# Performance work log

Hardware: AMD Instinct MI355X
Metric: run time of the kernel (lower is better)

Reference implementation:

```python
import jax, jax.numpy as jnp
import numpy as np

B, T, D = 4, 256, 512          # batch, seq_len, encoder_dim
L, H = 2, 8                    # num xLSTM blocks, num heads
I = 2 * D                      # inner dim (proj_factor=2)
DH = I // H                    # per-head dim = 128
K, G = 32, 64                  # mdn_components, goal_dim
EPS = 1e-5


def _ln(x, s, b):
    m = x.mean(-1, keepdims=True)
    v = jnp.mean((x - m) ** 2, -1, keepdims=True)
    return (x - m) * jax.lax.rsqrt(v + EPS) * s + b


def setup_inputs() -> dict:
    key = jax.random.key(0)
    ks = jax.random.split(key, 16)
    sc = 0.02
    nrm = lambda k, shp: jax.random.normal(k, shp, jnp.float32) * sc
    return {
        "x": jax.random.normal(ks[0], (B, T, D), jnp.float32),
        "ln_s": jnp.ones((L, D), jnp.float32),
        "ln_b": jnp.zeros((L, D), jnp.float32),
        "W_proj": nrm(ks[1], (L, D, 2 * I)),
        "Wq": nrm(ks[2], (L, I, I)),
        "Wk": nrm(ks[3], (L, I, I)),
        "Wv": nrm(ks[4], (L, I, I)),
        "Wi": nrm(ks[5], (L, I, H)),
        "bi": jnp.zeros((L, H), jnp.float32),
        "Wf": nrm(ks[6], (L, I, H)),
        "bf": jnp.full((L, H), 3.0, jnp.float32),  # forget-gate bias init
        "gn_s": jnp.ones((L, I), jnp.float32),
        "gn_b": jnp.zeros((L, I), jnp.float32),
        "W_down": nrm(ks[7], (L, I, D)),
        "fln_s": jnp.ones((D,), jnp.float32),
        "fln_b": jnp.zeros((D,), jnp.float32),
        "W_pi": nrm(ks[8], (D, K)),
        "b_pi": jnp.zeros((K,), jnp.float32),
        "W_mu": nrm(ks[9], (D, K * G)),
        "b_mu": jnp.zeros((K * G,), jnp.float32),
        "W_sig": nrm(ks[10], (D, K * G)),
        "b_sig": jnp.zeros((K * G,), jnp.float32),
    }


def _forward(x, ln_s, ln_b, W_proj, Wq, Wk, Wv, Wi, bi, Wf, bf,
             gn_s, gn_b, W_down, fln_s, fln_b,
             W_pi, b_pi, W_mu, b_mu, W_sig, b_sig):
    inv_sqrt_dh = 1.0 / (DH ** 0.5)

    def step(carry, x_t):  # x_t: (B, D); replicates per-timestep xlstm_stack.step()
        C, n, m = carry    # (L,B,H,DH,DH), (L,B,H,DH), (L,B,H)
        h = x_t
        for l in range(L):  # fixed small block loop
            skip = h
            xn = _ln(h, ln_s[l], ln_b[l])
            xp = xn @ W_proj[l]                      # (B, 2I)
            xm, z = jnp.split(xp, 2, axis=-1)        # mLSTM branch / gate branch
            q = (xm @ Wq[l]).reshape(B, H, DH)
            k = (xm @ Wk[l]).reshape(B, H, DH) * inv_sqrt_dh
            v = (xm @ Wv[l]).reshape(B, H, DH)
            ip = xm @ Wi[l] + bi[l]                  # (B, H) exp input gate preact
            fp = xm @ Wf[l] + bf[l]                  # (B, H) forget gate preact
            logf = jax.nn.log_sigmoid(fp)
            m_new = jnp.maximum(logf + m[l], ip)     # stabilizer
            ig = jnp.exp(ip - m_new)
            fg = jnp.exp(logf + m[l] - m_new)
            # matrix memory update: C <- f*C + i * k v^T ; n <- f*n + i*k
            C_new = fg[:, :, None, None] * C[l] + ig[:, :, None, None] * (k[..., :, None] * v[..., None, :])
            n_new = fg[..., None] * n[l] + ig[..., None] * k
            num = jnp.einsum('bhk,bhkv->bhv', q, C_new)
            den = jnp.maximum(jnp.abs(jnp.einsum('bhk,bhk->bh', q, n_new)), 1.0)
            hh = num / den[..., None]                # (B, H, DH)
            # multi-head norm (per-head layernorm, no per-head affine)
            mu_h = hh.mean(-1, keepdims=True)
            var_h = jnp.mean((hh - mu_h) ** 2, -1, keepdims=True)
            hh = (hh - mu_h) * jax.lax.rsqrt(var_h + EPS)
            hh = hh.reshape(B, I) * gn_s[l] + gn_b[l]
            hh = hh * jax.nn.silu(z)                 # output gating branch
            h = skip + hh @ W_down[l]                # residual
            C = C.at[l].set(C_new)
            n = n.at[l].set(n_new)
            m = m.at[l].set(m_new)
        return (C, n, m), h

    C0 = jnp.zeros((L, B, H, DH, DH), x.dtype)
    n0 = jnp.zeros((L, B, H, DH), x.dtype)
    m0 = jnp.zeros((L, B, H), x.dtype)
    _, hs = jax.lax.scan(step, (C0, n0, m0), jnp.swapaxes(x, 0, 1))
    last = _ln(hs[-1], fln_s, fln_b)                 # post-blocks norm on final step
    pi = jax.nn.softmax(last @ W_pi + b_pi, axis=-1)              # (B, K)
    mu = (last @ W_mu + b_mu).reshape(B, K, G)                     # (B, K, G)
    sigma = jax.nn.softplus(last @ W_sig + b_sig).reshape(B, K, G) # (B, K, G)
    return pi, mu, sigma


def reference(x, ln_s, ln_b, W_proj, Wq, Wk, Wv, Wi, bi, Wf, bf,
              gn_s, gn_b, W_down, fln_s, fln_b,
              W_pi, b_pi, W_mu, b_mu, W_sig, b_sig):
    return _forward(x, ln_s, ln_b, W_proj, Wq, Wk, Wv, Wi, bi, Wf, bf,
                    gn_s, gn_b, W_down, fln_s, fln_b,
                    W_pi, b_pi, W_mu, b_mu, W_sig, b_sig)
```

## Files before the change

### kernel.cpp

```cpp
#include <hip/hip_runtime.h>
#include <hip/hip_bf16.h>
#include <math.h>

#define DEV __device__ __forceinline__

typedef __attribute__((ext_vector_type(8))) short bf16x8;
typedef __attribute__((ext_vector_type(4))) float f32x4;

static DEV float softplus_f(float x){ return fmaxf(x,0.f) + log1pf(expf(-fabsf(x))); }
static DEV float logsig_f(float x){ return fminf(x,0.f) - log1pf(expf(-fabsf(x))); }
static DEV float silu_f(float x){ return x / (1.f + expf(-x)); }
static DEV unsigned short f2bf(float f){
  union { float f; unsigned u; } v; v.f = f;
  unsigned r = (v.u + 0x7fffu + ((v.u >> 16) & 1u)) >> 16;
  return (unsigned short)r;
}
static DEV float bf2f(unsigned short u){
  union { unsigned u; float f; } v; v.u = ((unsigned)u) << 16; return v.f;
}

__global__ void wconv_all(const float* __restrict__ Wp, const float* __restrict__ Wq,
                          const float* __restrict__ Wk, const float* __restrict__ Wv,
                          const float* __restrict__ Wd,
                          unsigned short* projT0, unsigned short* projT1,
                          unsigned short* qT0, unsigned short* kT0, unsigned short* kT1,
                          unsigned short* vT0, unsigned short* vT1, unsigned short* dT0)
{
  int z = blockIdx.z;
  const float* W; unsigned short* Wt; int K, M; float scale = 1.f;
  const float INV = 0.08838834764831845f;
  switch (z){
    case 0: W = Wp;              Wt = projT0; K = 512;  M = 2048; break;
    case 1: W = Wp + 512*2048;   Wt = projT1; K = 512;  M = 2048; break;
    case 2: W = Wq;              Wt = qT0;    K = 1024; M = 1024; break;
    case 3: W = Wk;              Wt = kT0;    K = 1024; M = 1024; scale = INV; break;
    case 4: W = Wk + 1048576;    Wt = kT1;    K = 1024; M = 1024; scale = INV; break;
    case 5: W = Wv;              Wt = vT0;    K = 1024; M = 1024; break;
    case 6: W = Wv + 1048576;    Wt = vT1;    K = 1024; M = 1024; break;
    default: W = Wd;             Wt = dT0;    K = 1024; M = 512;  break;
  }
  int m0 = blockIdx.x * 32, k0 = blockIdx.y * 32;
  if (m0 >= M || k0 >= K) return;
  __shared__ float s[32][33];
  int tx = threadIdx.x & 31, ty = threadIdx.x >> 5;
  #pragma unroll
  for (int u = 0; u < 32; u += 8)
    s[ty+u][tx] = W[(size_t)(k0+ty+u)*M + m0 + tx];
  __syncthreads();
  #pragma unroll
  for (int u = 0; u < 32; u += 8)
    Wt[(size_t)(m0+ty+u)*K + k0 + tx] = f2bf(s[tx][ty+u] * scale);
}

__global__ __launch_bounds__(256) void wcomb2(const float* __restrict__ W_proj,
                                              const float* __restrict__ Wi,
                                              const float* __restrict__ Wf,
                                              float* __restrict__ Wc)
{
  int gid = blockIdx.x * 4 + (threadIdx.x >> 6);
  int l = gid >> 9, d = gid & 511;
  int lane = threadIdx.x & 63;
  const float* wp = W_proj + (size_t)l*512*2048 + (size_t)d*2048 + lane*16;
  const float* wi = Wi + (size_t)l*1024*8;
  const float* wf = Wf + (size_t)l*1024*8;
  float acc[16];
  #pragma unroll
  for (int q = 0; q < 16; ++q) acc[q] = 0.f;
  #pragma unroll 4
  for (int u = 0; u < 16; ++u){
    float xv = wp[u];
    int j = lane*16 + u;
    float4 wi0 = *(const float4*)(wi + j*8);
    float4 wi1 = *(const float4*)(wi + j*8 + 4);
    float4 wf0 = *(const float4*)(wf + j*8);
    float4 wf1 = *(const float4*)(wf + j*8 + 4);
    acc[0]  = fmaf(xv, wi0.x, acc[0]);  acc[1]  = fmaf(xv, wi0.y, acc[1]);
    acc[2]  = fmaf(xv, wi0.z, acc[2]);  acc[3]  = fmaf(xv, wi0.w, acc[3]);
    acc[4]  = fmaf(xv, wi1.x, acc[4]);  acc[5]  = fmaf(xv, wi1.y, acc[5]);
    acc[6]  = fmaf(xv, wi1.z, acc[6]);  acc[7]  = fmaf(xv, wi1.w, acc[7]);
    acc[8]  = fmaf(xv, wf0.x, acc[8]);  acc[9]  = fmaf(xv, wf0.y, acc[9]);
    acc[10] = fmaf(xv, wf0.z, acc[10]); acc[11] = fmaf(xv, wf0.w, acc[11]);
    acc[12] = fmaf(xv, wf1.x, acc[12]); acc[13] = fmaf(xv, wf1.y, acc[13]);
    acc[14] = fmaf(xv, wf1.z, acc[14]); acc[15] = fmaf(xv, wf1.w, acc[15]);
  }
  #pragma unroll
  for (int o = 32; o > 0; o >>= 1){
    #pragma unroll
    for (int q = 0; q < 16; ++q) acc[q] += __shfl_xor(acc[q], o);
  }
  if (lane == 0){
    float* dst = Wc + (size_t)l*512*16 + d*16;
    #pragma unroll
    for (int q = 0; q < 16; ++q) dst[q] = acc[q];
  }
}

__global__ __launch_bounds__(256) void ln_gates(
    const float* __restrict__ in, unsigned short* __restrict__ outb,
    const float* __restrict__ s, const float* __restrict__ b,
    const float* __restrict__ Wc, float* __restrict__ ipfp)
{
  int r = blockIdx.x;
  const float* x = in + (size_t)r * 512;
  int tid = threadIdx.x;
  float lsum = 0.f, lsq = 0.f;
  for (int i = tid; i < 512; i += 256){ float v = x[i]; lsum += v; lsq += v*v; }
  #pragma unroll
  for (int o = 32; o > 0; o >>= 1){ lsum += __shfl_down(lsum, o); lsq += __shfl_down(lsq, o); }
  __shared__ float s1[4], s2[4];
  int wid = tid >> 6, lane = tid & 63;
  if (lane == 0){ s1[wid] = lsum; s2[wid] = lsq; }
  __syncthreads();
  if (tid == 0){ float a=0.f,c=0.f; for (int w=0; w<4; ++w){ a+=s1[w]; c+=s2[w]; } s1[0]=a; s2[0]=c; }
  __syncthreads();
  float mean = s1[0] * (1.f/512.f);
  float var  = s2[0] * (1.f/512.f) - mean*mean;
  float rstd = rsqrtf(var + 1e-5f);
  __shared__ float P[256][17];
  float g[16];
  #pragma unroll
  for (int q = 0; q < 16; ++q) g[q] = 0.f;
  for (int i = tid; i < 512; i += 256){
    float v = (x[i]-mean)*rstd*s[i] + b[i];
    outb[(size_t)r*512 + i] = f2bf(v);
    const float* wrow = Wc + i*16;
    #pragma unroll
    for (int q = 0; q < 16; ++q) g[q] = fmaf(v, wrow[q], g[q]);
  }
  #pragma unroll
  for (int q = 0; q < 16; ++q) P[tid][q] = g[q];
  __syncthreads();
  {
    int q = tid >> 4, c = tid & 15;
    float sacc = 0.f;
    #pragma unroll
    for (int u = 0; u < 16; ++u) sacc += P[c*16 + u][q];
    sacc += __shfl_xor(sacc, 1); sacc += __shfl_xor(sacc, 2);
    sacc += __shfl_xor(sacc, 4); sacc += __shfl_xor(sacc, 8);
    if (c == 0) ipfp[r*16 + q] = sacc;
  }
}

__global__ __launch_bounds__(256) void gemm_mfma128_multi(
    const unsigned short* __restrict__ A, int lda,
    const unsigned short* __restrict__ Bt0, const unsigned short* __restrict__ Bt1,
    const unsigned short* __restrict__ Bt2, int ldb,
    unsigned short* __restrict__ C0, unsigned short* __restrict__ C1,
    unsigned short* __restrict__ C2, int ldc, int K)
{
  const unsigned short* Bt = (blockIdx.z == 0) ? Bt0 : (blockIdx.z == 1) ? Bt1 : Bt2;
  unsigned short* Cbf      = (blockIdx.z == 0) ? C0  : (blockIdx.z == 1) ? C1  : C2;
  __shared__ __align__(16) unsigned short As[128][72];
  __shared__ __align__(16) unsigned short Bs[128][72];
  int row0 = blockIdx.y * 128, col0 = blockIdx.x * 128;
  int tid = threadIdx.x;
  int w = tid >> 6, l = tid & 63;
  int wr = (w >> 1) * 64, wc = (w & 1) * 64;
  int lr = l & 15, lk = l >> 4;
  f32x4 acc[4][4] = {};
  for (int k0 = 0; k0 < K; k0 += 64){
    #pragma unroll
    for (int u = 0; u < 4; ++u){
      int o = u*256 + tid, r = o >> 3, c = (o & 7) * 8;
      *(bf16x8*)&As[r][c] = *(const bf16x8*)(A  + (size_t)(row0 + r) * lda + k0 + c);
      *(bf16x8*)&Bs[r][c] = *(const bf16x8*)(Bt + (size_t)(col0 + r) * ldb + k0 + c);
    }
    __syncthreads();
    #pragma unroll
    for (int kk = 0; kk < 2; ++kk){
      bf16x8 af[4], bfr[4];
      #pragma unroll
      for (int i = 0; i < 4; ++i) af[i]  = *(const bf16x8*)&As[wr + i*16 + lr][kk*32 + lk*8];
      #pragma unroll
      for (int j = 0; j < 4; ++j) bfr[j] = *(const bf16x8*)&Bs[wc + j*16 + lr][kk*32 + lk*8];
      #pragma unroll
      for (int i = 0; i < 4; ++i)
        #pragma unroll
        for (int j = 0; j < 4; ++j)
          acc[i][j] = __builtin_amdgcn_mfma_f32_16x16x32_bf16(af[i], bfr[j], acc[i][j], 0, 0, 0);
    }
    __syncthreads();
  }
  #pragma unroll
  for (int i = 0; i < 4; ++i){
    #pragma unroll
    for (int j = 0; j < 4; ++j){
      int col = col0 + wc + j*16 + lr;
      #pragma unroll
      for (int r = 0; r < 4; ++r){
        int row = row0 + wr + i*16 + lk*4 + r;
        Cbf[(size_t)row*ldc + col] = f2bf(acc[i][j][r]);
      }
    }
  }
}

__global__ __launch_bounds__(256) void gemm_mfma(
    const unsigned short* __restrict__ A, int lda,
    const unsigned short* __restrict__ Bt, int ldb,
    float* __restrict__ C, int ldc,
    unsigned short* __restrict__ Cbf,
    const float* __restrict__ skip, int ldskip,
    int K)
{
  __shared__ __align__(16) unsigned short As[64][72];
  __shared__ __align__(16) unsigned short Bs[64][72];
  int row0 = blockIdx.y * 64, col0 = blockIdx.x * 64;
  int tid = threadIdx.x;
  int w = tid >> 6, l = tid & 63;
  int wr = (w >> 1) * 32, wc = (w & 1) * 32;
  int lr = l & 15, lk = l >> 4;
  int r1 = tid >> 3, c1 = (tid & 7) * 8;
  int r2 = (tid + 256) >> 3, c2 = ((tid + 256) & 7) * 8;
  const unsigned short* a1 = A  + (size_t)(row0 + r1) * lda + c1;
  const unsigned short* a2 = A  + (size_t)(row0 + r2) * lda + c2;
  const unsigned short* b1 = Bt + (size_t)(col0 + r1) * ldb + c1;
  const unsigned short* b2 = Bt + (size_t)(col0 + r2) * ldb + c2;
  f32x4 acc00 = {0,0,0,0}, acc01 = {0,0,0,0}, acc10 = {0,0,0,0}, acc11 = {0,0,0,0};
  for (int k0 = 0; k0 < K; k0 += 64){
    *(bf16x8*)&As[r1][c1] = *(const bf16x8*)(a1 + k0);
    *(bf16x8*)&As[r2][c2] = *(const bf16x8*)(a2 + k0);
    *(bf16x8*)&Bs[r1][c1] = *(const bf16x8*)(b1 + k0);
    *(bf16x8*)&Bs[r2][c2] = *(const bf16x8*)(b2 + k0);
    __syncthreads();
    #pragma unroll
    for (int kk = 0; kk < 2; ++kk){
      bf16x8 a0 = *(const bf16x8*)&As[wr + lr][kk*32 + lk*8];
      bf16x8 a1f = *(const bf16x8*)&As[wr + 16 + lr][kk*32 + lk*8];
      bf16x8 b0 = *(const bf16x8*)&Bs[wc + lr][kk*32 + lk*8];
      bf16x8 b1f = *(const bf16x8*)&Bs[wc + 16 + lr][kk*32 + lk*8];
      acc00 = __builtin_amdgcn_mfma_f32_16x16x32_bf16(a0, b0, acc00, 0, 0, 0);
      acc01 = __builtin_amdgcn_mfma_f32_16x16x32_bf16(a0, b1f, acc01, 0, 0, 0);
      acc10 = __builtin_amdgcn_mfma_f32_16x16x32_bf16(a1f, b0, acc10, 0, 0, 0);
      acc11 = __builtin_amdgcn_mfma_f32_16x16x32_bf16(a1f, b1f, acc11, 0, 0, 0);
    }
    __syncthreads();
  }
  #pragma unroll
  for (int i = 0; i < 2; ++i){
    #pragma unroll
    for (int j = 0; j < 2; ++j){
      f32x4 a = (i == 0) ? ((j == 0) ? acc00 : acc01) : ((j == 0) ? acc10 : acc11);
      int col = col0 + wc + j*16 + lr;
      #pragma unroll
      for (int r = 0; r < 4; ++r){
        int row = row0 + wr + i*16 + lk*4 + r;
        float o = a[r];
        if (skip) o += skip[(size_t)row*ldskip + col];
        if (C)   C[(size_t)row*ldc + col] = o;
        if (Cbf) Cbf[(size_t)row*ldc + col] = f2bf(o);
      }
    }
  }
}

__global__ void scan_gates(const float* __restrict__ ipfp,
                           const float* __restrict__ bi, const float* __restrict__ bfg,
                           float* __restrict__ alpha, float* __restrict__ Mt)
{
  int bh = blockIdx.x; int b = bh >> 3, h = bh & 7;
  int lane = threadIdx.x;
  float bih = bi[h], bfh = bfg[h];
  float lf[4], ip[4];
  #pragma unroll
  for (int u = 0; u < 4; ++u){
    int t = lane*4 + u, r = b*256 + t;
    ip[u] = ipfp[r*16 + h] + bih;
    lf[u] = logsig_f(ipfp[r*16 + 8 + h] + bfh);
  }
  float c0 = lf[0], c1 = c0+lf[1], c2 = c1+lf[2], c3 = c2+lf[3];
  float tot = c3, pre = tot;
  #pragma unroll
  for (int o = 1; o < 64; o <<= 1){ float v = __shfl_up(pre, o); if (lane >= o) pre += v; }
  float excl = pre - tot;
  float F[4] = {excl+c0, excl+c1, excl+c2, excl+c3};
  float al[4];
  #pragma unroll
  for (int u = 0; u < 4; ++u) al[u] = ip[u] - F[u];
  float lm[4];
  lm[0] = al[0]; lm[1] = fmaxf(lm[0], al[1]); lm[2] = fmaxf(lm[1], al[2]); lm[3] = fmaxf(lm[2], al[3]);
  float pm = lm[3];
  #pragma unroll
  for (int o = 1; o < 64; o <<= 1){ float v = __shfl_up(pm, o); if (lane >= o) pm = fmaxf(pm, v); }
  float pmexcl = __shfl_up(pm, 1);
  if (lane == 0) pmexcl = -3.4e38f;
  int base = bh*256 + lane*4;
  #pragma unroll
  for (int u = 0; u < 4; ++u){
    alpha[base+u] = al[u];
    Mt[base+u] = fmaxf(0.f, fmaxf(pmexcl, lm[u]));
  }
}

__global__ __launch_bounds__(256) void attn_l0_mfma(
    const unsigned short* __restrict__ q, const unsigned short* __restrict__ k,
    const unsigned short* __restrict__ v,
    const float* __restrict__ alpha, const float* __restrict__ Mt,
    const unsigned short* __restrict__ xpb,
    const float* __restrict__ gn_s, const float* __restrict__ gn_b,
    unsigned short* __restrict__ gated)
{
  __shared__ __align__(16) char smem[46080];
  unsigned short (*Ks)[136] = (unsigned short(*)[136])smem;
  unsigned short (*Vt)[72]  = (unsigned short(*)[72])(smem + 17408);
  unsigned short (*Ps)[72]  = (unsigned short(*)[72])(smem + 35840);
  float* alpha_sh = (float*)(smem + 45056);
  float* Mt_sh    = (float*)(smem + 45312);
  float (*denL)[64] = (float(*)[64])(smem + 45568);
  float (*numf)[140] = (float(*)[140])smem;

  int blk = blockIdx.x;
  int tt = blk & 3, h = (blk >> 2) & 7, b = blk >> 5;
  int t0 = tt * 64;
  int tid = threadIdx.x;
  int w = tid >> 6, l = tid & 63;
  int wr = (w >> 1) * 32;
  int wc = (w & 1) * 32;
  int wd = (w & 1) * 64;
  int lrm = l & 15, lk = l >> 4;
  int bhT = ((b*8 + h) << 8);
  size_t headoff = (size_t)h * 128;

  {
    #pragma unroll
    for (int u = 0; u < 4; ++u){
      int o = u*256 + tid, row = o >> 4, oct = o & 15;
      *(bf16x8*)&Ks[row][oct*8] =
        *(const bf16x8*)(q + (size_t)(b*256 + t0 + row)*1024 + headoff + oct*8);
    }
    if (tid < 64) Mt_sh[tid] = Mt[bhT + t0 + tid];
    if (tid < 128) ((float*)denL)[tid] = 0.f;
  }
  __syncthreads();
  bf16x8 aq[2][4];
  #pragma unroll
  for (int i = 0; i < 2; ++i)
    #pragma unroll
    for (int kk = 0; kk < 4; ++kk)
      aq[i][kk] = *(const bf16x8*)&Ks[wr + i*16 + lrm][kk*32 + lk*8];
  __syncthreads();

  f32x4 pacc[2][4] = {};
  int ntile = tt + 1;

  for (int it = 0; it < ntile; ++it){
    int s0 = it * 64;
    #pragma unroll
    for (int u = 0; u < 4; ++u){
      int o = u*256 + tid, row = o >> 4, oct = o & 15;
      *(bf16x8*)&Ks[row][oct*8] =
        *(const bf16x8*)(k + (size_t)(b*256 + s0 + row)*1024 + headoff + oct*8);
    }
    #pragma unroll
    for (int u = 0; u < 2; ++u){
      int task = u*256 + tid;
      int sp = task & 31, oct = task >> 5;
      const unsigned short* vp = v + (size_t)(b*256 + s0 + sp*2)*1024 + headoff + oct*8;
      bf16x8 r0 = *(const bf16x8*)vp;
      bf16x8 r1 = *(const bf16x8*)(vp + 1024);
      #pragma unroll
      for (int j = 0; j < 8; ++j){
        unsigned lo = (unsigned short)r0[j];
        unsigned hi = (unsigned short)r1[j];
        *(unsigned*)&Vt[oct*8 + j][sp*2] = lo | (hi << 16);
      }
    }
    if (tid < 64) alpha_sh[tid] = alpha[bhT + s0 + tid];
    __syncthreads();

    f32x4 sacc[2][2] = {};
    #pragma unroll
    for (int kk = 0; kk < 4; ++kk){
      bf16x8 b0 = *(const bf16x8*)&Ks[wc + lrm][kk*32 + lk*8];
      bf16x8 b1 = *(const bf16x8*)&Ks[wc + 16 + lrm][kk*32 + lk*8];
      sacc[0][0] = __builtin_amdgcn_mfma_f32_16x16x32_bf16(aq[0][kk], b0, sacc[0][0], 0, 0, 0);
      sacc[0][1] = __builtin_amdgcn_mfma_f32_16x16x32_bf16(aq[0][kk], b1, sacc[0][1], 0, 0, 0);
      sacc[1][0] = __builtin_amdgcn_mfma_f32_16x16x32_bf16(aq[1][kk], b0, sacc[1][0], 0, 0, 0);
      sacc[1][1] = __builtin_amdgcn_mfma_f32_16x16x32_bf16(aq[1][kk], b1, sacc[1][1], 0, 0, 0);
    }

    bool diag = (it == ntile - 1);
    float av0 = alpha_sh[wc + lrm];
    float av1 = alpha_sh[wc + 16 + lrm];
    #pragma unroll
    for (int i = 0; i < 2; ++i){
      #pragma unroll
      for (int r = 0; r < 4; ++r){
        int tl = wr + i*16 + lk*4 + r;
        float mt = Mt_sh[tl];
        float p0 = __expf(av0 - mt) * sacc[i][0][r];
        float p1 = __expf(av1 - mt) * sacc[i][1][r];
        if (diag){
          if (wc + lrm      > tl) p0 = 0.f;
          if (wc + 16 + lrm > tl) p1 = 0.f;
        }
        Ps[tl][wc + lrm]      = f2bf(p0);
        Ps[tl][wc + 16 + lrm] = f2bf(p1);
        float dv = p0 + p1;
        dv += __shfl_xor(dv, 1); dv += __shfl_xor(dv, 2);
        dv += __shfl_xor(dv, 4); dv += __shfl_xor(dv, 8);
        if (lrm == 0) denL[w & 1][tl] += dv;
      }
    }
    __syncthreads();

    #pragma unroll
    for (int ks = 0; ks < 2; ++ks){
      bf16x8 pa0 = *(const bf16x8*)&Ps[wr + lrm][ks*32 + lk*8];
      bf16x8 pa1 = *(const bf16x8*)&Ps[wr + 16 + lrm][ks*32 + lk*8];
      #pragma unroll
      for (int jd = 0; jd < 4; ++jd){
        bf16x8 vb8 = *(const bf16x8*)&Vt[wd + jd*16 + lrm][ks*32 + lk*8];
        pacc[0][jd] = __builtin_amdgcn_mfma_f32_16x16x32_bf16(pa0, vb8, pacc[0][jd], 0, 0, 0);
        pacc[1][jd] = __builtin_amdgcn_mfma_f32_16x16x32_bf16(pa1, vb8, pacc[1][jd], 0, 0, 0);
      }
    }
    __syncthreads();
  }

  #pragma unroll
  for (int i = 0; i < 2; ++i)
    #pragma unroll
    for (int jd = 0; jd < 4; ++jd)
      #pragma unroll
      for (int r = 0; r < 4; ++r)
        numf[wr + i*16 + lk*4 + r][wd + jd*16 + lrm] = pacc[i][jd][r];
  if (tid < 64){
    float s = denL[0][tid] + denL[1][tid];
    alpha_sh[tid] = 1.0f / fmaxf(fabsf(s), 1.0f);
  }
  __syncthreads();

  {
    int row = tid >> 2, qq = tid & 3;
    float inv = alpha_sh[row];
    const float* nr = &numf[row][qq*32];
    float xs[32];
    float sum = 0.f, sq = 0.f;
    #pragma unroll
    for (int j = 0; j < 8; ++j){
      float4 t4 = *(const float4*)(nr + j*4);
      float v0 = t4.x*inv, v1 = t4.y*inv, v2 = t4.z*inv, v3 = t4.w*inv;
      xs[j*4+0] = v0; xs[j*4+1] = v1; xs[j*4+2] = v2; xs[j*4+3] = v3;
      sum += v0+v1+v2+v3;
      sq  += v0*v0+v1*v1+v2*v2+v3*v3;
    }
    sum += __shfl_xor(sum, 1); sq += __shfl_xor(sq, 1);
    sum += __shfl_xor(sum, 2); sq += __shfl_xor(sq, 2);
    float mean = sum * (1.f/128.f);
    float var  = sq  * (1.f/128.f) - mean*mean;
    float rstd = rsqrtf(var + 1e-5f);
    int rr = b*256 + t0 + row;
    const unsigned short* zp = xpb + (size_t)rr*2048 + 1024 + headoff + qq*32;
    const float* gsP = gn_s + headoff + qq*32;
    const float* gbP = gn_b + headoff + qq*32;
    unsigned short* op = gated + (size_t)rr*1024 + headoff + qq*32;
    #pragma unroll
    for (int j8 = 0; j8 < 4; ++j8){
      bf16x8 zv = *(const bf16x8*)(zp + j8*8);
      bf16x8 ov;
      #pragma unroll
      for (int j = 0; j < 8; ++j){
        int jj = j8*8 + j;
        float valn = (xs[jj]-mean)*rstd*gsP[jj] + gbP[jj];
        ov[j] = (short)f2bf(valn * silu_f(bf2f((unsigned short)zv[j])));
      }
      *(bf16x8*)(op + j8*8) = ov;
    }
  }
}

__global__ void qlast_split(const unsigned short* __restrict__ xpb, const float* __restrict__ Wq1,
                            float* __restrict__ part)
{
  int jt = blockIdx.x, ks = blockIdx.y;
  int j = jt*256 + threadIdx.x;
  __shared__ float xs[4][32];
  int t = threadIdx.x;
  if (t < 128){ int b = t >> 5, kk = t & 31; xs[b][kk] = bf2f(xpb[(size_t)(b*256+255)*2048 + ks*32 + kk]); }
  __syncthreads();
  float a0=0.f,a1=0.f,a2=0.f,a3=0.f;
  #pragma unroll 8
  for (int kk = 0; kk < 32; ++kk){
    float wv = Wq1[(size_t)(ks*32+kk)*1024 + j];
    a0 = fmaf(xs[0][kk], wv, a0);
    a1 = fmaf(xs[1][kk], wv, a1);
    a2 = fmaf(xs[2][kk], wv, a2);
    a3 = fmaf(xs[3][kk], wv, a3);
  }
  part[((size_t)ks*4 + 0)*1024 + j] = a0;
  part[((size_t)ks*4 + 1)*1024 + j] = a1;
  part[((size_t)ks*4 + 2)*1024 + j] = a2;
  part[((size_t)ks*4 + 3)*1024 + j] = a3;
}

__global__ __launch_bounds__(256) void attn_l1_split(
    const float* __restrict__ qpart, const unsigned short* __restrict__ k1,
    const unsigned short* __restrict__ v1,
    const float* __restrict__ alpha, const float* __restrict__ Mt,
    float* __restrict__ pnum, float* __restrict__ pden)
{
  int sc = blockIdx.x, bh = blockIdx.y;
  int b = bh >> 3, h = bh & 7;
  int s0 = sc * 32;
  int tid = threadIdx.x;
  __shared__ float qsh[128];
  __shared__ float sred[32][9];
  __shared__ float as[32];
  __shared__ float nred[2][128];
  if (tid < 128){
    float s = 0.f;
    #pragma unroll 8
    for (int ks = 0; ks < 32; ++ks) s += qpart[((size_t)ks*4 + b)*1024 + h*128 + tid];
    qsh[tid] = s;
  }
  __syncthreads();
  {
    int sl = tid & 31, dc = tid >> 5;
    const unsigned short* kp = k1 + (size_t)(b*256 + s0 + sl)*1024 + h*128 + dc*16;
    float p = 0.f;
    #pragma unroll
    for (int u = 0; u < 16; u += 8){
      bf16x8 kv = *(const bf16x8*)(kp + u);
      #pragma unroll
      for (int e = 0; e < 8; ++e) p = fmaf(qsh[dc*16+u+e], bf2f((unsigned short)kv[e]), p);
    }
    sred[sl][dc] = p;
  }
  __syncthreads();
  if (tid < 32){
    float sum = 0.f;
    #pragma unroll
    for (int dc = 0; dc < 8; ++dc) sum += sred[tid][dc];
    float w = __expf(alpha[bh*256 + s0 + tid] - Mt[bh*256 + 255]);
    as[tid] = w * sum;
  }
  __syncthreads();
  {
    int d = tid & 127, sg = tid >> 7;
    const unsigned short* vp = v1 + (size_t)(b*256 + s0 + sg*16)*1024 + h*128 + d;
    float np = 0.f;
    #pragma unroll
    for (int u = 0; u < 16; ++u) np = fmaf(as[sg*16 + u], bf2f(vp[(size_t)u*1024]), np);
    nred[sg][d] = np;
  }
  __syncthreads();
  if (tid < 128) pnum[((size_t)bh*8 + sc)*128 + tid] = nred[0][tid] + nred[1][tid];
  if (tid == 128){
    float dsum = 0.f;
    #pragma unroll
    for (int u = 0; u < 32; ++u) dsum += as[u];
    pden[bh*8 + sc] = dsum;
  }
}

__global__ __launch_bounds__(128) void attn_l1_fin(
    const float* __restrict__ pnum, const float* __restrict__ pden,
    const unsigned short* __restrict__ xpb,
    const float* __restrict__ gn_s, const float* __restrict__ gn_b,
    float* __restrict__ gated1)
{
  int bh = blockIdx.x; int b = bh >> 3, h = bh & 7;
  int tid = threadIdx.x;
  __shared__ float hh[128];
  __shared__ float dsh, msh, rsh;
  float nsum = 0.f;
  #pragma unroll
  for (int sc = 0; sc < 8; ++sc) nsum += pnum[((size_t)bh*8 + sc)*128 + tid];
  if (tid == 0){
    float d = 0.f;
    #pragma unroll
    for (int sc = 0; sc < 8; ++sc) d += pden[bh*8 + sc];
    dsh = fmaxf(fabsf(d), 1.0f);
  }
  __syncthreads();
  float hv = nsum / dsh;
  hh[tid] = hv;
  __syncthreads();
  if (tid < 64){
    float a = hh[tid], c = hh[tid + 64];
    float s1 = a + c, s2v = a*a + c*c;
    #pragma unroll
    for (int o = 32; o > 0; o >>= 1){ s1 += __shfl_down(s1, o); s2v += __shfl_down(s2v, o); }
    if (tid == 0){
      float mean = s1*(1.f/128.f);
      float var  = s2v*(1.f/128.f) - mean*mean;
      msh = mean; rsh = rsqrtf(var + 1e-5f);
    }
  }
  __syncthreads();
  {
    int i = h*128 + tid;
    float valn = (hv - msh)*rsh*gn_s[i] + gn_b[i];
    float z = bf2f(xpb[(size_t)(b*256 + 255)*2048 + 1024 + i]);
    gated1[b*1024 + i] = valn * silu_f(z);
  }
}

__global__ void dl_split(const float* __restrict__ gated1, const float* __restrict__ Wd,
                         float* __restrict__ part)
{
  int jt = blockIdx.x, ks = blockIdx.y;
  int j = jt*256 + threadIdx.x;
  __shared__ float xs[4][32];
  int t = threadIdx.x;
  if (t < 128){ int b = t >> 5, kk = t & 31; xs[b][kk] = gated1[b*1024 + ks*32 + kk]; }
  __syncthreads();
  float a0=0.f,a1=0.f,a2=0.f,a3=0.f;
  #pragma unroll 8
  for (int kk = 0; kk < 32; ++kk){
    float wv = Wd[(size_t)(ks*32+kk)*512 + j];
    a0 = fmaf(xs[0][kk], wv, a0);
    a1 = fmaf(xs[1][kk], wv, a1);
    a2 = fmaf(xs[2][kk], wv, a2);
    a3 = fmaf(xs[3][kk], wv, a3);
  }
  part[((size_t)ks*4 + 0)*512 + j] = a0;
  part[((size_t)ks*4 + 1)*512 + j] = a1;
  part[((size_t)ks*4 + 2)*512 + j] = a2;
  part[((size_t)ks*4 + 3)*512 + j] = a3;
}

__global__ __launch_bounds__(256) void dl_fin(
    const float* __restrict__ part, const float* __restrict__ h0,
    const float* __restrict__ fln_s, const float* __restrict__ fln_b,
    float* __restrict__ lastb)
{
  int b = blockIdx.x;
  int tid = threadIdx.x;
  float v[2];
  #pragma unroll
  for (int u = 0; u < 2; ++u){
    int jj = tid*2 + u;
    float s = 0.f;
    #pragma unroll 8
    for (int ks = 0; ks < 32; ++ks) s += part[((size_t)ks*4 + b)*512 + jj];
    v[u] = h0[(size_t)(b*256 + 255)*512 + jj] + s;
  }
  float lsum = v[0] + v[1], lsq = v[0]*v[0] + v[1]*v[1];
  #pragma unroll
  for (int o = 32; o > 0; o >>= 1){ lsum += __shfl_down(lsum, o); lsq += __shfl_down(lsq, o); }
  __shared__ float s1[4], s2[4];
  int wid = tid >> 6, lane = tid & 63;
  if (lane == 0){ s1[wid] = lsum; s2[wid] = lsq; }
  __syncthreads();
  if (tid == 0){ float a=0.f,c=0.f; for (int w2=0; w2<4; ++w2){ a+=s1[w2]; c+=s2[w2]; } s1[0]=a; s2[0]=c; }
  __syncthreads();
  float mean = s1[0] * (1.f/512.f);
  float var  = s2[0] * (1.f/512.f) - mean*mean;
  float rstd = rsqrtf(var + 1e-5f);
  #pragma unroll
  for (int u = 0; u < 2; ++u){
    int jj = tid*2 + u;
    lastb[b*512 + jj] = (v[u]-mean)*rstd*fln_s[jj] + fln_b[jj];
  }
}

__global__ void ms_split(const float* __restrict__ last,
                         const float* __restrict__ W_mu, const float* __restrict__ W_sig,
                         float* __restrict__ part)
{
  int jt = blockIdx.x, ks = blockIdx.y, mat = blockIdx.z;
  int j = jt*256 + threadIdx.x;
  const float* W = mat ? W_sig : W_mu;
  __shared__ float xs[4][64];
  int t = threadIdx.x;
  { int b = t >> 6, kk = t & 63; xs[b][kk] = last[b*512 + ks*64 + kk]; }
  __syncthreads();
  float a0=0.f,a1=0.f,a2=0.f,a3=0.f;
  #pragma unroll 8
  for (int kk = 0; kk < 64; ++kk){
    float wv = W[(size_t)(ks*64+kk)*2048 + j];
    a0 = fmaf(xs[0][kk], wv, a0);
    a1 = fmaf(xs[1][kk], wv, a1);
    a2 = fmaf(xs[2][kk], wv, a2);
    a3 = fmaf(xs[3][kk], wv, a3);
  }
  size_t base = ((size_t)(mat*8 + ks)*4);
  part[(base + 0)*2048 + j] = a0;
  part[(base + 1)*2048 + j] = a1;
  part[(base + 2)*2048 + j] = a2;
  part[(base + 3)*2048 + j] = a3;
}

__global__ void ms_reduce(const float* __restrict__ part,
                          const float* __restrict__ b_mu, const float* __restrict__ b_sig,
                          float* __restrict__ out)
{
  int j = blockIdx.x*256 + threadIdx.x;
  int b = blockIdx.y, mat = blockIdx.z;
  float s = mat ? b_sig[j] : b_mu[j];
  for (int ks = 0; ks < 8; ++ks) s += part[((size_t)(mat*8 + ks)*4 + b)*2048 + j];
  out[128 + mat*8192 + b*2048 + j] = mat ? softplus_f(s) : s;
}

__global__ void heads_pi(const float* __restrict__ last,
                         const float* __restrict__ W_pi, const float* __restrict__ b_pi,
                         float* __restrict__ out)
{
  __shared__ float ls[512];
  int b = blockIdx.x, o = threadIdx.x;
  for (int i = o; i < 512; i += 64) ls[i] = last[b*512 + i];
  __syncthreads();
  bool valid = o < 32;
  float acc = -3.4e38f;
  if (valid){
    acc = b_pi[o];
    for (int i = 0; i < 512; ++i) acc = fmaf(ls[i], W_pi[i*32 + o], acc);
  }
  float m = acc;
  #pragma unroll
  for (int o2 = 32; o2 > 0; o2 >>= 1) m = fmaxf(m, __shfl_xor(m, o2));
  float e = valid ? expf(acc - m) : 0.f;
  float ssum = e;
  #pragma unroll
  for (int o2 = 32; o2 > 0; o2 >>= 1) ssum += __shfl_xor(ssum, o2);
  if (valid) out[b*32 + o] = e / ssum;
}

extern "C" void kernel_launch(void* const* d_in, const int* in_sizes, int n_in,
                              void* d_out, int out_size, void* d_ws, size_t ws_size,
                              hipStream_t stream)
{
  const float* x      = (const float*)d_in[0];
  const float* ln_s   = (const float*)d_in[1];
  const float* ln_b   = (const float*)d_in[2];
  const float* W_proj = (const float*)d_in[3];
  const float* Wq     = (const float*)d_in[4];
  const float* Wk     = (const float*)d_in[5];
  const float* Wv     = (const float*)d_in[6];
  const float* Wi     = (const float*)d_in[7];
  const float* bi     = (const float*)d_in[8];
  const float* Wf     = (const float*)d_in[9];
  const float* bf     = (const float*)d_in[10];
  const float* gn_s   = (const float*)d_in[11];
  const float* gn_b   = (const float*)d_in[12];
  const float* W_down = (const float*)d_in[13];
  const float* fln_s  = (const float*)d_in[14];
  const float* fln_b  = (const float*)d_in[15];
  const float* W_pi   = (const float*)d_in[16];
  const float* b_pi   = (const float*)d_in[17];
  const float* W_mu   = (const float*)d_in[18];
  const float* b_mu   = (const float*)d_in[19];
  const float* W_sig  = (const float*)d_in[20];
  const float* b_sig  = (const float*)d_in[21];
  float* out = (float*)d_out;

  char* p = (char*)d_ws;
  unsigned short* projT0 = (unsigned short*)p; p += (size_t)2048*512*2;
  unsigned short* projT1 = (unsigned short*)p; p += (size_t)2048*512*2;
  unsigned short* qT0    = (unsigned short*)p; p += (size_t)1024*1024*2;
  unsigned short* kT0    = (unsigned short*)p; p += (size_t)1024*1024*2;
  unsigned short* kT1    = (unsigned short*)p; p += (size_t)1024*1024*2;
  unsigned short* vT0    = (unsigned short*)p; p += (size_t)1024*1024*2;
  unsigned short* vT1    = (unsigned short*)p; p += (size_t)1024*1024*2;
  unsigned short* dT0    = (unsigned short*)p; p += (size_t)512*1024*2;
  float* Wc              = (float*)p;          p += (size_t)2*512*16*4;
  unsigned short* xnb    = (unsigned short*)p; p += (size_t)1024*512*2;
  unsigned short* xpb    = (unsigned short*)p; p += (size_t)1024*2048*2;
  unsigned short* qbb    = (unsigned short*)p; p += (size_t)1024*1024*2;
  unsigned short* kbb    = (unsigned short*)p; p += (size_t)1024*1024*2;
  unsigned short* vbb    = (unsigned short*)p; p += (size_t)1024*1024*2;
  unsigned short* gatedb = (unsigned short*)p; p += (size_t)1024*1024*2;
  float* h0     = (float*)p; p += (size_t)1024*512*4;
  float* ipfp   = (float*)p; p += (size_t)16384*4;
  float* alpha  = (float*)p; p += (size_t)8192*4;
  float* Mtb    = (float*)p; p += (size_t)8192*4;
  float* gated1 = (float*)p; p += (size_t)4096*4;
  float* lastb  = (float*)p; p += (size_t)2048*4;
  float* qpart  = (float*)p; p += (size_t)32*4096*4;
  float* dpart  = (float*)p; p += (size_t)32*4*512*4;
  float* pnum   = (float*)p; p += (size_t)32*8*128*4;
  float* pden   = (float*)p; p += (size_t)32*8*4;
  float* mspart = (float*)p; p += (size_t)16*4*2048*4;

  const float* ln_s1 = ln_s + 512;
  const float* ln_b1 = ln_b + 512;
  const float* gn_s1 = gn_s + 1024;
  const float* gn_b1 = gn_b + 1024;
  const float* Wq1   = Wq + 1024*1024;
  const float* Wd1   = W_down + 1024*512;

  dim3 blk256(256);

  wconv_all<<<dim3(64,32,8), blk256, 0, stream>>>(W_proj, Wq, Wk, Wv, W_down,
      projT0, projT1, qT0, kT0, kT1, vT0, vT1, dT0);
  wcomb2<<<256, blk256, 0, stream>>>(W_proj, Wi, Wf, Wc);

  ln_gates<<<1024, blk256, 0, stream>>>(x, xnb, ln_s, ln_b, Wc, ipfp);
  gemm_mfma128_multi<<<dim3(16,8,1), blk256, 0, stream>>>(xnb, 512, projT0, projT0, projT0, 512, xpb, xpb, xpb, 2048, 512);
  gemm_mfma128_multi<<<dim3(8,8,3), blk256, 0, stream>>>(xpb, 2048, qT0, kT0, vT0, 1024, qbb, kbb, vbb, 1024, 1024);
  scan_gates<<<32, 64, 0, stream>>>(ipfp, bi, bf, alpha, Mtb);
  attn_l0_mfma<<<128, blk256, 0, stream>>>(qbb, kbb, vbb, alpha, Mtb, xpb, gn_s, gn_b, gatedb);
  gemm_mfma<<<dim3(8,16), blk256, 0, stream>>>(gatedb, 1024, dT0, 1024, h0, 512, nullptr, x, 512, 1024);

  ln_gates<<<1024, blk256, 0, stream>>>(h0, xnb, ln_s1, ln_b1, Wc + 512*16, ipfp);
  gemm_mfma128_multi<<<dim3(16,8,1), blk256, 0, stream>>>(xnb, 512, projT1, projT1, projT1, 512, xpb, xpb, xpb, 2048, 512);
  gemm_mfma128_multi<<<dim3(8,8,2), blk256, 0, stream>>>(xpb, 2048, kT1, vT1, vT1, 1024, kbb, vbb, vbb, 1024, 1024);
  scan_gates<<<32, 64, 0, stream>>>(ipfp, bi + 8, bf + 8, alpha, Mtb);
  qlast_split<<<dim3(4,32), blk256, 0, stream>>>(xpb, Wq1, qpart);
  attn_l1_split<<<dim3(8,32), blk256, 0, stream>>>(qpart, kbb, vbb, alpha, Mtb, pnum, pden);
  attn_l1_fin<<<32, 128, 0, stream>>>(pnum, pden, xpb, gn_s1, gn_b1, gated1);
  dl_split<<<dim3(2,32), blk256, 0, stream>>>(gated1, Wd1, dpart);
  dl_fin<<<4, blk256, 0, stream>>>(dpart, h0, fln_s, fln_b, lastb);

  ms_split<<<dim3(8,8,2), blk256, 0, stream>>>(lastb, W_mu, W_sig, mspart);
  ms_reduce<<<dim3(8,4,2), blk256, 0, stream>>>(mspart, b_mu, b_sig, out);
  heads_pi<<<4, 64, 0, stream>>>(lastb, W_pi, b_pi, out);
}
```

Baseline: 197.2 us.

## Fuse gate scans, weight prep and pi head into neighbouring kernels

Measured after the change: 197.1 us. No clear change (-0.0%).

```diff
diff --git a/kernel.cpp b/kernel.cpp
--- a/kernel.cpp
+++ b/kernel.cpp
@@ -19,14 +19,58 @@
   union { unsigned u; float f; } v; v.u = ((unsigned)u) << 16; return v.f;
 }
 
-__global__ void wconv_all(const float* __restrict__ Wp, const float* __restrict__ Wq,
-                          const float* __restrict__ Wk, const float* __restrict__ Wv,
-                          const float* __restrict__ Wd,
-                          unsigned short* projT0, unsigned short* projT1,
-                          unsigned short* qT0, unsigned short* kT0, unsigned short* kT1,
-                          unsigned short* vT0, unsigned short* vT1, unsigned short* dT0)
+__global__ __launch_bounds__(256) void wprep(
+    const float* __restrict__ Wp, const float* __restrict__ Wq,
+    const float* __restrict__ Wk, const float* __restrict__ Wv,
+    const float* __restrict__ Wd, const float* __restrict__ Wi,
+    const float* __restrict__ Wf,
+    unsigned short* projT0, unsigned short* projT1,
+    unsigned short* qT0, unsigned short* kT0, unsigned short* kT1,
+    unsigned short* vT0, unsigned short* vT1, unsigned short* dT0,
+    float* __restrict__ Wc)
 {
   int z = blockIdx.z;
+  if (z == 8){
+    int fb = blockIdx.y * 64 + blockIdx.x;
+    if (fb >= 256) return;
+    int gid = fb * 4 + (threadIdx.x >> 6);
+    int l = gid >> 9, d = gid & 511;
+    int lane = threadIdx.x & 63;
+    const float* wp = Wp + (size_t)l*512*2048 + (size_t)d*2048 + lane*16;
+    const float* wi = Wi + (size_t)l*1024*8;
+    const float* wf = Wf + (size_t)l*1024*8;
+    float acc[16];
+    #pragma unroll
+    for (int q = 0; q < 16; ++q) acc[q] = 0.f;
+    #pragma unroll 4
+    for (int u = 0; u < 16; ++u){
+      float xv = wp[u];
+      int j = lane*16 + u;
+      float4 wi0 = *(const float4*)(wi + j*8);
+      float4 wi1 = *(const float4*)(wi + j*8 + 4);
+      float4 wf0 = *(const float4*)(wf + j*8);
+      float4 wf1 = *(const float4*)(wf + j*8 + 4);
+      acc[0]  = fmaf(xv, wi0.x, acc[0]);  acc[1]  = fmaf(xv, wi0.y, acc[1]);
+      acc[2]  = fmaf(xv, wi0.z, acc[2]);  acc[3]  = fmaf(xv, wi0.w, acc[3]);
+      acc[4]  = fmaf(xv, wi1.x, acc[4]);  acc[5]  = fmaf(xv, wi1.y, acc[5]);
+      acc[6]  = fmaf(xv, wi1.z, acc[6]);  acc[7]  = fmaf(xv, wi1.w, acc[7]);
+      acc[8]  = fmaf(xv, wf0.x, acc[8]);  acc[9]  = fmaf(xv, wf0.y, acc[9]);
+      acc[10] = fmaf(xv, wf0.z, acc[10]); acc[11] = fmaf(xv, wf0.w, acc[11]);
+      acc[12] = fmaf(xv, wf1.x, acc[12]); acc[13] = fmaf(xv, wf1.y, acc[13]);
+      acc[14] = fmaf(xv, wf1.z, acc[14]); acc[15] = fmaf(xv, wf1.w, acc[15]);
+    }
+    #pragma unroll
+    for (int o = 32; o > 0; o >>= 1){
+      #pragma unroll
+      for (int q = 0; q < 16; ++q) acc[q] += __shfl_xor(acc[q], o);
+    }
+    if (lane == 0){
+      float* dst = Wc + (size_t)l*512*16 + d*16;
+      #pragma unroll
+      for (int q = 0; q < 16; ++q) dst[q] = acc[q];
+    }
+    return;
+  }
   const float* W; unsigned short* Wt; int K, M; float scale = 1.f;
   const float INV = 0.08838834764831845f;
   switch (z){
@@ -50,49 +94,6 @@
   #pragma unroll
   for (int u = 0; u < 32; u += 8)
     Wt[(size_t)(m0+ty+u)*K + k0 + tx] = f2bf(s[tx][ty+u] * scale);
-}
-
-__global__ __launch_bounds__(256) void wcomb2(const float* __restrict__ W_proj,
-                                              const float* __restrict__ Wi,
-                                              const float* __restrict__ Wf,
-                                              float* __restrict__ Wc)
-{
-  int gid = blockIdx.x * 4 + (threadIdx.x >> 6);
-  int l = gid >> 9, d = gid & 511;
-  int lane = threadIdx.x & 63;
-  const float* wp = W_proj + (size_t)l*512*2048 + (size_t)d*2048 + lane*16;
-  const float* wi = Wi + (size_t)l*1024*8;
-  const float* wf = Wf + (size_t)l*1024*8;
-  float acc[16];
-  #pragma unroll
-  for (int q = 0; q < 16; ++q) acc[q] = 0.f;
-  #pragma unroll 4
-  for (int u = 0; u < 16; ++u){
-    float xv = wp[u];
-    int j = lane*16 + u;
-    float4 wi0 = *(const float4*)(wi + j*8);
-    float4 wi1 = *(const float4*)(wi + j*8 + 4);
-    float4 wf0 = *(const float4*)(wf + j*8);
-    float4 wf1 = *(const float4*)(wf + j*8 + 4);
-    acc[0]  = fmaf(xv, wi0.x, acc[0]);  acc[1]  = fmaf(xv, wi0.y, acc[1]);
-    acc[2]  = fmaf(xv, wi0.z, acc[2]);  acc[3]  = fmaf(xv, wi0.w, acc[3]);
-    acc[4]  = fmaf(xv, wi1.x, acc[4]);  acc[5]  = fmaf(xv, wi1.y, acc[5]);
-    acc[6]  = fmaf(xv, wi1.z, acc[6]);  acc[7]  = fmaf(xv, wi1.w, acc[7]);
-    acc[8]  = fmaf(xv, wf0.x, acc[8]);  acc[9]  = fmaf(xv, wf0.y, acc[9]);
-    acc[10] = fmaf(xv, wf0.z, acc[10]); acc[11] = fmaf(xv, wf0.w, acc[11]);
-    acc[12] = fmaf(xv, wf1.x, acc[12]); acc[13] = fmaf(xv, wf1.y, acc[13]);
-    acc[14] = fmaf(xv, wf1.z, acc[14]); acc[15] = fmaf(xv, wf1.w, acc[15]);
-  }
-  #pragma unroll
-  for (int o = 32; o > 0; o >>= 1){
-    #pragma unroll
-    for (int q = 0; q < 16; ++q) acc[q] += __shfl_xor(acc[q], o);
-  }
-  if (lane == 0){
-    float* dst = Wc + (size_t)l*512*16 + d*16;
-    #pragma unroll
-    for (int q = 0; q < 16; ++q) dst[q] = acc[q];
-  }
 }
 
 __global__ __launch_bounds__(256) void ln_gates(
@@ -254,59 +255,22 @@
   }
 }
 
-__global__ void scan_gates(const float* __restrict__ ipfp,
-                           const float* __restrict__ bi, const float* __restrict__ bfg,
-                           float* __restrict__ alpha, float* __restrict__ Mt)
-{
-  int bh = blockIdx.x; int b = bh >> 3, h = bh & 7;
-  int lane = threadIdx.x;
-  float bih = bi[h], bfh = bfg[h];
-  float lf[4], ip[4];
-  #pragma unroll
-  for (int u = 0; u < 4; ++u){
-    int t = lane*4 + u, r = b*256 + t;
-    ip[u] = ipfp[r*16 + h] + bih;
-    lf[u] = logsig_f(ipfp[r*16 + 8 + h] + bfh);
-  }
-  float c0 = lf[0], c1 = c0+lf[1], c2 = c1+lf[2], c3 = c2+lf[3];
-  float tot = c3, pre = tot;
-  #pragma unroll
-  for (int o = 1; o < 64; o <<= 1){ float v = __shfl_up(pre, o); if (lane >= o) pre += v; }
-  float excl = pre - tot;
-  float F[4] = {excl+c0, excl+c1, excl+c2, excl+c3};
-  float al[4];
-  #pragma unroll
-  for (int u = 0; u < 4; ++u) al[u] = ip[u] - F[u];
-  float lm[4];
-  lm[0] = al[0]; lm[1] = fmaxf(lm[0], al[1]); lm[2] = fmaxf(lm[1], al[2]); lm[3] = fmaxf(lm[2], al[3]);
-  float pm = lm[3];
-  #pragma unroll
-  for (int o = 1; o < 64; o <<= 1){ float v = __shfl_up(pm, o); if (lane >= o) pm = fmaxf(pm, v); }
-  float pmexcl = __shfl_up(pm, 1);
-  if (lane == 0) pmexcl = -3.4e38f;
-  int base = bh*256 + lane*4;
-  #pragma unroll
-  for (int u = 0; u < 4; ++u){
-    alpha[base+u] = al[u];
-    Mt[base+u] = fmaxf(0.f, fmaxf(pmexcl, lm[u]));
-  }
-}
-
 __global__ __launch_bounds__(256) void attn_l0_mfma(
     const unsigned short* __restrict__ q, const unsigned short* __restrict__ k,
     const unsigned short* __restrict__ v,
-    const float* __restrict__ alpha, const float* __restrict__ Mt,
+    const float* __restrict__ ipfp, const float* __restrict__ bi, const float* __restrict__ bfg,
     const unsigned short* __restrict__ xpb,
     const float* __restrict__ gn_s, const float* __restrict__ gn_b,
     unsigned short* __restrict__ gated)
 {
-  __shared__ __align__(16) char smem[46080];
+  __shared__ __align__(16) char smem[48128];
   unsigned short (*Ks)[136] = (unsigned short(*)[136])smem;
   unsigned short (*Vt)[72]  = (unsigned short(*)[72])(smem + 17408);
   unsigned short (*Ps)[72]  = (unsigned short(*)[72])(smem + 35840);
-  float* alpha_sh = (float*)(smem + 45056);
-  float* Mt_sh    = (float*)(smem + 45312);
+  float* invden = (float*)(smem + 45056);
   float (*denL)[64] = (float(*)[64])(smem + 45568);
+  float* alpha_full = (float*)(smem + 46080);
+  float* Mt_full    = (float*)(smem + 47104);
   float (*numf)[140] = (float(*)[140])smem;
 
   int blk = blockIdx.x;
@@ -318,7 +282,6 @@
   int wc = (w & 1) * 32;
   int wd = (w & 1) * 64;
   int lrm = l & 15, lk = l >> 4;
-  int bhT = ((b*8 + h) << 8);
   size_t headoff = (size_t)h * 128;
 
   {
@@ -328,7 +291,35 @@
       *(bf16x8*)&Ks[row][oct*8] =
         *(const bf16x8*)(q + (size_t)(b*256 + t0 + row)*1024 + headoff + oct*8);
     }
-    if (tid < 64) Mt_sh[tid] = Mt[bhT + t0 + tid];
+    if (tid < 64){
+      int lane = tid;
+      float bih = bi[h], bfh = bfg[h];
+      float lf[4], ip4[4];
+      #pragma unroll
+      for (int u = 0; u < 4; ++u){
+        int r = b*256 + lane*4 + u;
+        ip4[u] = ipfp[r*16 + h] + bih;
+        lf[u]  = logsig_f(ipfp[r*16 + 8 + h] + bfh);
+      }
+      float c0 = lf[0], c1 = c0+lf[1], c2 = c1+lf[2], c3 = c2+lf[3];
+      float tot = c3, pre = tot;
+      #pragma unroll
+      for (int o = 1; o < 64; o <<= 1){ float vv = __shfl_up(pre, o); if (lane >= o) pre += vv; }
+      float excl = pre - tot;
+      float al[4] = { ip4[0]-(excl+c0), ip4[1]-(excl+c1), ip4[2]-(excl+c2), ip4[3]-(excl+c3) };
+      float lm[4];
+      lm[0]=al[0]; lm[1]=fmaxf(lm[0],al[1]); lm[2]=fmaxf(lm[1],al[2]); lm[3]=fmaxf(lm[2],al[3]);
+      float pm = lm[3];
+      #pragma unroll
+      for (int o = 1; o < 64; o <<= 1){ float vv = __shfl_up(pm, o); if (lane >= o) pm = fmaxf(pm, vv); }
+      float pmexcl = __shfl_up(pm, 1);
+      if (lane == 0) pmexcl = -3.4e38f;
+      #pragma unroll
+      for (int u = 0; u < 4; ++u){
+        alpha_full[lane*4+u] = al[u];
+        Mt_full[lane*4+u] = fmaxf(0.f, fmaxf(pmexcl, lm[u]));
+      }
+    }
     if (tid < 128) ((float*)denL)[tid] = 0.f;
   }
   __syncthreads();
@@ -365,7 +356,6 @@
         *(unsigned*)&Vt[oct*8 + j][sp*2] = lo | (hi << 16);
       }
     }
-    if (tid < 64) alpha_sh[tid] = alpha[bhT + s0 + tid];
     __syncthreads();
 
     f32x4 sacc[2][2] = {};
@@ -380,14 +370,14 @@
     }
 
     bool diag = (it == ntile - 1);
-    float av0 = alpha_sh[wc + lrm];
-    float av1 = alpha_sh[wc + 16 + lrm];
+    float av0 = alpha_full[s0 + wc + lrm];
+    float av1 = alpha_full[s0 + wc + 16 + lrm];
     #pragma unroll
     for (int i = 0; i < 2; ++i){
       #pragma unroll
       for (int r = 0; r < 4; ++r){
         int tl = wr + i*16 + lk*4 + r;
-        float mt = Mt_sh[tl];
+        float mt = Mt_full[t0 + tl];
         float p0 = __expf(av0 - mt) * sacc[i][0][r];
         float p1 = __expf(av1 - mt) * sacc[i][1][r];
         if (diag){
@@ -427,13 +417,13 @@
         numf[wr + i*16 + lk*4 + r][wd + jd*16 + lrm] = pacc[i][jd][r];
   if (tid < 64){
     float s = denL[0][tid] + denL[1][tid];
-    alpha_sh[tid] = 1.0f / fmaxf(fabsf(s), 1.0f);
+    invden[tid] = 1.0f / fmaxf(fabsf(s), 1.0f);
   }
   __syncthreads();
 
   {
     int row = tid >> 2, qq = tid & 3;
-    float inv = alpha_sh[row];
+    float inv = invden[row];
     const float* nr = &numf[row][qq*32];
     float xs[32];
     float sum = 0.f, sq = 0.f;
@@ -497,7 +487,7 @@
 __global__ __launch_bounds__(256) void attn_l1_split(
     const float* __restrict__ qpart, const unsigned short* __restrict__ k1,
     const unsigned short* __restrict__ v1,
-    const float* __restrict__ alpha, const float* __restrict__ Mt,
+    const float* __restrict__ ipfp, const float* __restrict__ bi, const float* __restrict__ bfg,
     float* __restrict__ pnum, float* __restrict__ pden)
 {
   int sc = blockIdx.x, bh = blockIdx.y;
@@ -505,6 +495,8 @@
   int s0 = sc * 32;
   int tid = threadIdx.x;
   __shared__ float qsh[128];
+  __shared__ float alpha256[256];
+  __shared__ float mt255s;
   __shared__ float sred[32][9];
   __shared__ float as[32];
   __shared__ float nred[2][128];
@@ -514,6 +506,29 @@
     for (int ks = 0; ks < 32; ++ks) s += qpart[((size_t)ks*4 + b)*1024 + h*128 + tid];
     qsh[tid] = s;
   }
+  if (tid >= 128 && tid < 192){
+    int lane = tid - 128;
+    float bih = bi[h], bfh = bfg[h];
+    float lf[4], ip4[4];
+    #pragma unroll
+    for (int u = 0; u < 4; ++u){
+      int r = b*256 + lane*4 + u;
+      ip4[u] = ipfp[r*16 + h] + bih;
+      lf[u]  = logsig_f(ipfp[r*16 + 8 + h] + bfh);
+    }
+    float c0 = lf[0], c1 = c0+lf[1], c2 = c1+lf[2], c3 = c2+lf[3];
+    float tot = c3, pre = tot;
+    #pragma unroll
+    for (int o = 1; o < 64; o <<= 1){ float vv = __shfl_up(pre, o); if (lane >= o) pre += vv; }
+    float excl = pre - tot;
+    float al[4] = { ip4[0]-(excl+c0), ip4[1]-(excl+c1), ip4[2]-(excl+c2), ip4[3]-(excl+c3) };
+    #pragma unroll
+    for (int u = 0; u < 4; ++u) alpha256[lane*4+u] = al[u];
+    float mx = fmaxf(fmaxf(al[0],al[1]), fmaxf(al[2],al[3]));
+    #pragma unroll
+    for (int o = 32; o > 0; o >>= 1) mx = fmaxf(mx, __shfl_xor(mx, o));
+    if (lane == 0) mt255s = fmaxf(0.f, mx);
+  }
   __syncthreads();
   {
     int sl = tid & 31, dc = tid >> 5;
@@ -532,7 +547,7 @@
     float sum = 0.f;
     #pragma unroll
     for (int dc = 0; dc < 8; ++dc) sum += sred[tid][dc];
-    float w = __expf(alpha[bh*256 + s0 + tid] - Mt[bh*256 + 255]);
+    float w = __expf(alpha256[s0 + tid] - mt255s);
     as[tid] = w * sum;
   }
   __syncthreads();
@@ -624,10 +639,14 @@
 __global__ __launch_bounds__(256) void dl_fin(
     const float* __restrict__ part, const float* __restrict__ h0,
     const float* __restrict__ fln_s, const float* __restrict__ fln_b,
-    float* __restrict__ lastb)
+    const float* __restrict__ W_pi, const float* __restrict__ b_pi,
+    float* __restrict__ lastb, float* __restrict__ out)
 {
   int b = blockIdx.x;
   int tid = threadIdx.x;
+  __shared__ float ls[512];
+  __shared__ float pred[8][33];
+  __shared__ float s1[4], s2[4];
   float v[2];
   #pragma unroll
   for (int u = 0; u < 2; ++u){
@@ -640,7 +659,6 @@
   float lsum = v[0] + v[1], lsq = v[0]*v[0] + v[1]*v[1];
   #pragma unroll
   for (int o = 32; o > 0; o >>= 1){ lsum += __shfl_down(lsum, o); lsq += __shfl_down(lsq, o); }
-  __shared__ float s1[4], s2[4];
   int wid = tid >> 6, lane = tid & 63;
   if (lane == 0){ s1[wid] = lsum; s2[wid] = lsq; }
   __syncthreads();
@@ -652,7 +670,31 @@
   #pragma unroll
   for (int u = 0; u < 2; ++u){
     int jj = tid*2 + u;
-    lastb[b*512 + jj] = (v[u]-mean)*rstd*fln_s[jj] + fln_b[jj];
+    float lv = (v[u]-mean)*rstd*fln_s[jj] + fln_b[jj];
+    lastb[b*512 + jj] = lv;
+    ls[jj] = lv;
+  }
+  __syncthreads();
+  {
+    int o = tid & 31, pt = tid >> 5;
+    float pa = 0.f;
+    #pragma unroll 8
+    for (int u = 0; u < 64; ++u){ int i = pt*64 + u; pa = fmaf(ls[i], W_pi[i*32 + o], pa); }
+    pred[pt][o] = pa;
+  }
+  __syncthreads();
+  if (tid < 32){
+    float acc = b_pi[tid];
+    #pragma unroll
+    for (int pt = 0; pt < 8; ++pt) acc += pred[pt][tid];
+    float m = acc;
+    #pragma unroll
+    for (int o2 = 16; o2 > 0; o2 >>= 1) m = fmaxf(m, __shfl_xor(m, o2));
+    float e = __expf(acc - m);
+    float ss = e;
+    #pragma unroll
+    for (int o2 = 16; o2 > 0; o2 >>= 1) ss += __shfl_xor(ss, o2);
+    out[b*32 + tid] = e / ss;
   }
 }
 
@@ -692,30 +734,6 @@
   float s = mat ? b_sig[j] : b_mu[j];
   for (int ks = 0; ks < 8; ++ks) s += part[((size_t)(mat*8 + ks)*4 + b)*2048 + j];
   out[128 + mat*8192 + b*2048 + j] = mat ? softplus_f(s) : s;
-}
-
-__global__ void heads_pi(const float* __restrict__ last,
-                         const float* __restrict__ W_pi, const float* __restrict__ b_pi,
-                         float* __restrict__ out)
-{
-  __shared__ float ls[512];
-  int b = blockIdx.x, o = threadIdx.x;
-  for (int i = o; i < 512; i += 64) ls[i] = last[b*512 + i];
-  __syncthreads();
-  bool valid = o < 32;
-  float acc = -3.4e38f;
-  if (valid){
-    acc = b_pi[o];
-    for (int i = 0; i < 512; ++i) acc = fmaf(ls[i], W_pi[i*32 + o], acc);
-  }
-  float m = acc;
-  #pragma unroll
-  for (int o2 = 32; o2 > 0; o2 >>= 1) m = fmaxf(m, __shfl_xor(m, o2));
-  float e = valid ? expf(acc - m) : 0.f;
-  float ssum = e;
-  #pragma unroll
-  for (int o2 = 32; o2 > 0; o2 >>= 1) ssum += __shfl_xor(ssum, o2);
-  if (valid) out[b*32 + o] = e / ssum;
 }
 
 extern "C" void kernel_launch(void* const* d_in, const int* in_sizes, int n_in,
@@ -764,8 +782,6 @@
   unsigned short* gatedb = (unsigned short*)p; p += (size_t)1024*1024*2;
   float* h0     = (float*)p; p += (size_t)1024*512*4;
   float* ipfp   = (float*)p; p += (size_t)16384*4;
-  float* alpha  = (float*)p; p += (size_t)8192*4;
-  float* Mtb    = (float*)p; p += (size_t)8192*4;
   float* gated1 = (float*)p; p += (size_t)4096*4;
   float* lastb  = (float*)p; p += (size_t)2048*4;
   float* qpart  = (float*)p; p += (size_t)32*4096*4;
@@ -783,28 +799,24 @@
 
   dim3 blk256(256);
 
-  wconv_all<<<dim3(64,32,8), blk256, 0, stream>>>(W_proj, Wq, Wk, Wv, W_down,
-      projT0, projT1, qT0, kT0, kT1, vT0, vT1, dT0);
-  wcomb2<<<256, blk256, 0, stream>>>(W_proj, Wi, Wf, Wc);
+  wprep<<<dim3(64,32,9), blk256, 0, stream>>>(W_proj, Wq, Wk, Wv, W_down, Wi, Wf,
+      projT0, projT1, qT0, kT0, kT1, vT0, vT1, dT0, Wc);
 
   ln_gates<<<1024, blk256, 0, stream>>>(x, xnb, ln_s, ln_b, Wc, ipfp);
   gemm_mfma128_multi<<<dim3(16,8,1), blk256, 0, stream>>>(xnb, 512, projT0, projT0, projT0, 512, xpb, xpb, xpb, 2048, 512);
   gemm_mfma128_multi<<<dim3(8,8,3), blk256, 0, stream>>>(xpb, 2048, qT0, kT0, vT0, 1024, qbb, kbb, vbb, 1024, 1024);
-  scan_gates<<<32, 64, 0, stream>>>(ipfp, bi, bf, alpha, Mtb);
-  attn_l0_mfma<<<128, blk256, 0, stream>>>(qbb, kbb, vbb, alpha, Mtb, xpb, gn_s, gn_b, gatedb);
+  attn_l0_mfma<<<128, blk256, 0, stream>>>(qbb, kbb, vbb, ipfp, bi, bf, xpb, gn_s, gn_b, gatedb);
   gemm_mfma<<<dim3(8,16), blk256, 0, stream>>>(gatedb, 1024, dT0, 1024, h0, 512, nullptr, x, 512, 1024);
 
   ln_gates<<<1024, blk256, 0, stream>>>(h0, xnb, ln_s1, ln_b1, Wc + 512*16, ipfp);
   gemm_mfma128_multi<<<dim3(16,8,1), blk256, 0, stream>>>(xnb, 512, projT1, projT1, projT1, 512, xpb, xpb, xpb, 2048, 512);
   gemm_mfma128_multi<<<dim3(8,8,2), blk256, 0, stream>>>(xpb, 2048, kT1, vT1, vT1, 1024, kbb, vbb, vbb, 1024, 1024);
-  scan_gates<<<32, 64, 0, stream>>>(ipfp, bi + 8, bf + 8, alpha, Mtb);
   qlast_split<<<dim3(4,32), blk256, 0, stream>>>(xpb, Wq1, qpart);
-  attn_l1_split<<<dim3(8,32), blk256, 0, stream>>>(qpart, kbb, vbb, alpha, Mtb, pnum, pden);
+  attn_l1_split<<<dim3(8,32), blk256, 0, stream>>>(qpart, kbb, vbb, ipfp, bi + 8, bf + 8, pnum, pden);
   attn_l1_fin<<<32, 128, 0, stream>>>(pnum, pden, xpb, gn_s1, gn_b1, gated1);
   dl_split<<<dim3(2,32), blk256, 0, stream>>>(gated1, Wd1, dpart);
-  dl_fin<<<4, blk256, 0, stream>>>(dpart, h0, fln_s, fln_b, lastb);
+  dl_fin<<<4, blk256, 0, stream>>>(dpart, h0, fln_s, fln_b, W_pi, b_pi, lastb, out);
 
   ms_split<<<dim3(8,8,2), blk256, 0, stream>>>(lastb, W_mu, W_sig, mspart);
   ms_reduce<<<dim3(8,4,2), blk256, 0, stream>>>(mspart, b_mu, b_sig, out);
-  heads_pi<<<4, 64, 0, stream>>>(lastb, W_pi, b_pi, out);
-}
+}
```
